# Kernel tuning notes

Measured on AMD Instinct MI355X. Metric: run time of the kernel, lower is better.

The kernel has to match this reference:

```python
import jax, jax.numpy as jnp
import numpy as np

NUM_HEADS = 8
QWH, QWW = 8, 8
KWH, KWW = 8, 8

def _relative_position_index():
    # Swin-style relative position index, exactly as in build()
    ch, cw = np.arange(QWH), np.arange(QWW)
    cq = np.stack(np.meshgrid(ch, cw, indexing='ij')).reshape(2, -1)  # [2, qN]
    ch, cw = np.arange(KWH), np.arange(KWW)
    ck = np.stack(np.meshgrid(ch, cw, indexing='ij')).reshape(2, -1)  # [2, kN]
    rel = (cq[:, :, None] - ck[:, None, :]).transpose(1, 2, 0)        # [qN, kN, 2]
    rel[:, :, 0] += KWH - 1
    rel[:, :, 1] += KWW - 1
    rel[:, :, 0] *= QWW + KWW - 1
    return rel.sum(-1)  # [qN, kN] int

_REL_IDX = jnp.asarray(_relative_position_index())

def setup_inputs() -> dict:
    key = jax.random.key(0)
    k1, k2, k3, k4 = jax.random.split(key, 4)
    B, C = 2048, 256
    q = jax.random.normal(k1, (B, QWH, QWW, C), dtype=jnp.float32)
    k = jax.random.normal(k2, (B, KWH, KWW, C), dtype=jnp.float32)
    v = jax.random.normal(k3, (B, KWH, KWW, C), dtype=jnp.float32)
    num_elements = (QWH + KWH - 1) * (QWW + KWW - 1)  # 225
    bias_table = 0.02 * jax.random.truncated_normal(
        k4, -2.0, 2.0, (num_elements, NUM_HEADS), dtype=jnp.float32)
    return {"q": q, "k": k, "v": v, "bias_table": bias_table}

def reference(q, k, v, bias_table):
    B, qWh, qWw, C = q.shape
    _, kWh, kWw, _ = k.shape
    qN, kN = qWh * qWw, kWh * kWw
    H = NUM_HEADS
    d = C // H
    scale = d ** -0.5
    # [B, N, H, d] -> [B, H, N, d]
    qh = q.reshape(B, qN, H, d).transpose(0, 2, 1, 3) * scale
    kh = k.reshape(B, kN, H, d).transpose(0, 2, 1, 3)
    vh = v.reshape(B, kN, H, d).transpose(0, 2, 1, 3)
    attn = jnp.einsum('bhqd,bhkd->bhqk', qh, kh)
    # gather relative-position bias: [qN, kN, H] -> [1, H, qN, kN]
    bias = bias_table[_REL_IDX].transpose(2, 0, 1)[None]
    attn = jax.nn.softmax(attn + bias, axis=-1)
    # bhqk,bhkd -> bqhd then merge heads back to channels
    x = jnp.einsum('bhqk,bhkd->bqhd', attn, vh).reshape(B, qWh, qWw, C)
    return x, attn
```

## Files before the change

kernel.cpp:

```cpp
#include <hip/hip_runtime.h>


#define NUM_HEADS 8

typedef __attribute__((ext_vector_type(8))) short bf16x8;
typedef __attribute__((ext_vector_type(4))) float f32x4;

__device__ inline unsigned cvt_pk_bf16(float lo, float hi) {
    unsigned r;
    asm("v_cvt_pk_bf16_f32 %0, %1, %2" : "=v"(r) : "v"(lo), "v"(hi));
    return r;
}

__global__ __launch_bounds__(256) void spatial_attn_mfma(
    const float* __restrict__ q,
    const float* __restrict__ k,
    const float* __restrict__ v,
    const float* __restrict__ bias_table,
    float* __restrict__ x_out,
    float* __restrict__ attn_out)
{
    __shared__ short q_lds[64 * 32];
    __shared__ short k_lds[64 * 32];
    __shared__ short vt_lds[32 * 64];
    __shared__ short p_lds[64 * 64];
    __shared__ float attn_lds[64 * 64];
    __shared__ float bias_s[225];

    const int bh  = blockIdx.x;
    const int b   = bh >> 3;
    const int h   = bh & 7;
    const int tid = threadIdx.x;
    const int lane = tid & 63;
    const int w    = tid >> 6;

    constexpr float LOG2E  = 1.4426950408889634f;
    constexpr float SCALE2 = 0.17677669529663687f * 1.4426950408889634f;
    const size_t base = ((size_t)b * 64) * 256 + h * 32;

    #pragma unroll
    for (int it = 0; it < 2; ++it) {
        const int i   = tid + it * 256;
        const int r   = i >> 3;
        const int d4  = (i & 7) * 4;
        const size_t off = base + (size_t)r * 256 + d4;
        const f32x4 qv = __builtin_nontemporal_load((const f32x4*)(q + off));
        const f32x4 kv = __builtin_nontemporal_load((const f32x4*)(k + off));
        const f32x4 vv = __builtin_nontemporal_load((const f32x4*)(v + off));

        const int u  = d4 >> 3;
        const int so = r * 32 + ((u ^ ((r >> 1) & 3)) << 3) + (d4 & 7);
        uint2 qb, kb;
        qb.x = cvt_pk_bf16(qv[0] * SCALE2, qv[1] * SCALE2);
        qb.y = cvt_pk_bf16(qv[2] * SCALE2, qv[3] * SCALE2);
        kb.x = cvt_pk_bf16(kv[0], kv[1]);
        kb.y = cvt_pk_bf16(kv[2], kv[3]);
        *(uint2*)(&q_lds[so]) = qb;
        *(uint2*)(&k_lds[so]) = kb;

        const unsigned vb0 = cvt_pk_bf16(vv[0], vv[1]);
        const unsigned vb1 = cvt_pk_bf16(vv[2], vv[3]);
        const int ur = r >> 3, rl = r & 7;
        vt_lds[(d4+0)*64 + ((ur ^ ((d4+0)&7)) << 3) + rl] = (short)vb0;
        vt_lds[(d4+1)*64 + ((ur ^ ((d4+1)&7)) << 3) + rl] = (short)(vb0 >> 16);
        vt_lds[(d4+2)*64 + ((ur ^ ((d4+2)&7)) << 3) + rl] = (short)vb1;
        vt_lds[(d4+3)*64 + ((ur ^ ((d4+3)&7)) << 3) + rl] = (short)(vb1 >> 16);
    }
    for (int i = tid; i < 225; i += 256)
        bias_s[i] = bias_table[i * NUM_HEADS + h] * LOG2E;
    __syncthreads();

    const int lr = lane & 15;
    const int lg = lane >> 4;
    const int arow = 16 * w + lr;
    const bf16x8 a_frag =
        *(const bf16x8*)(&q_lds[arow * 32 + ((lg ^ ((arow >> 1) & 3)) << 3)]);

    const int crow_base = 16 * w + lg * 4;

    f32x4 acc[4];
    {
        const int lrh = lr >> 3, lrl = lr & 7;
        #pragma unroll
        for (int j = 0; j < 4; ++j) {
            const int e  = 4 * lg + j;
            const int bj = (2 * w + (e >> 3) - lrh + 7) * 15 + (e & 7) - lrl + 7;
            #pragma unroll
            for (int t = 0; t < 4; ++t) acc[t][j] = bias_s[bj - 30 * t];
        }
    }
    #pragma unroll
    for (int t = 0; t < 4; ++t) {
        const int krow = 16 * t + lr;
        const bf16x8 b_frag =
            *(const bf16x8*)(&k_lds[krow * 32 + ((lg ^ ((krow >> 1) & 3)) << 3)]);
        acc[t] = __builtin_amdgcn_mfma_f32_16x16x32_bf16(a_frag, b_frag, acc[t], 0, 0, 0);
    }

    #pragma unroll
    for (int j = 0; j < 4; ++j) {
        const int rr = crow_base + j;
        float e0 = __builtin_amdgcn_exp2f(acc[0][j]);
        float e1 = __builtin_amdgcn_exp2f(acc[1][j]);
        float e2 = __builtin_amdgcn_exp2f(acc[2][j]);
        float e3 = __builtin_amdgcn_exp2f(acc[3][j]);
        float s = (e0 + e1) + (e2 + e3);
        s += __shfl_xor(s, 1);
        s += __shfl_xor(s, 2);
        s += __shfl_xor(s, 4);
        s += __shfl_xor(s, 8);
        const float inv = __builtin_amdgcn_rcpf(s);
        e0 *= inv; e1 *= inv; e2 *= inv; e3 *= inv;

        const int rb64 = rr * 64, rot = 4 * rr;
        attn_lds[rb64 + ((lr      + rot) & 63)] = e0;
        attn_lds[rb64 + ((16 + lr + rot) & 63)] = e1;
        attn_lds[rb64 + ((32 + lr + rot) & 63)] = e2;
        attn_lds[rb64 + ((48 + lr + rot) & 63)] = e3;

        const unsigned p01 = cvt_pk_bf16(e0, e1);
        const unsigned p23 = cvt_pk_bf16(e2, e3);
        const int rsw = rr & 7, rb = rr * 64, cl = lr & 7, ch = (lr >> 3);
        p_lds[rb + (((0 + ch) ^ rsw) << 3) + cl] = (short)p01;
        p_lds[rb + (((2 + ch) ^ rsw) << 3) + cl] = (short)(p01 >> 16);
        p_lds[rb + (((4 + ch) ^ rsw) << 3) + cl] = (short)p23;
        p_lds[rb + (((6 + ch) ^ rsw) << 3) + cl] = (short)(p23 >> 16);
    }

    const size_t attn_base = (size_t)bh * 64 * 64;
    #pragma unroll
    for (int j2 = 0; j2 < 4; ++j2) {
        const int rr = 16 * w + 4 * j2 + (lane >> 4);
        const int c0 = 4 * (lane & 15);
        const f32x4 av = *(const f32x4*)(&attn_lds[rr * 64 + ((c0 + 4 * rr) & 63)]);
        __builtin_nontemporal_store(av,
            (f32x4*)(attn_out + attn_base + (size_t)rr * 64 + c0));
    }

    f32x4 o[2] = {};
    const int prow = 16 * w + lr;
    #pragma unroll
    for (int s = 0; s < 2; ++s) {
        const int unit = s * 4 + lg;
        const bf16x8 pa =
            *(const bf16x8*)(&p_lds[prow * 64 + ((unit ^ (prow & 7)) << 3)]);
        #pragma unroll
        for (int t = 0; t < 2; ++t) {
            const int c = 16 * t + lr;
            const bf16x8 vb =
                *(const bf16x8*)(&vt_lds[c * 64 + ((unit ^ (c & 7)) << 3)]);
            o[t] = __builtin_amdgcn_mfma_f32_16x16x32_bf16(pa, vb, o[t], 0, 0, 0);
        }
    }

    {
        float* xs = attn_lds + 16 * w * 64;
        #pragma unroll
        for (int t = 0; t < 2; ++t) {
            #pragma unroll
            for (int j = 0; j < 4; ++j) {
                const int rr = crow_base + j;
                xs[(rr & 15) * 32 + ((16 * t + lr + 4 * rr) & 31)] = o[t][j];
            }
        }
        #pragma unroll
        for (int j3 = 0; j3 < 2; ++j3) {
            const int rr = 16 * w + 8 * j3 + (lane >> 3);
            const int c0 = 4 * (lane & 7);
            const f32x4 xv = *(const f32x4*)(&xs[(rr & 15) * 32 + ((c0 + 4 * rr) & 31)]);
            __builtin_nontemporal_store(xv,
                (f32x4*)(x_out + base + (size_t)rr * 256 + c0));
        }
    }
}

extern "C" void kernel_launch(void* const* d_in, const int* in_sizes, int n_in,
                              void* d_out, int out_size, void* d_ws, size_t ws_size,
                              hipStream_t stream) {
    const float* q    = (const float*)d_in[0];
    const float* k    = (const float*)d_in[1];
    const float* v    = (const float*)d_in[2];
    const float* bias = (const float*)d_in[3];

    const int B = in_sizes[0] / (8 * 8 * 256);
    float* x_out    = (float*)d_out;
    float* attn_out = x_out + (size_t)B * 64 * 256;

    spatial_attn_mfma<<<dim3(B * NUM_HEADS), dim3(256), 0, stream>>>(
        q, k, v, bias, x_out, attn_out);
}
```

Baseline: 159.9 us.

## Shrink LDS footprint, load Q fragments directly, reuse shared buffer for staging

Drops the Q and attn LDS buffers. Each lane now loads its own Q MFMA A-fragment from global memory and converts it to bf16 in registers. Softmax results stay in the accumulator registers and are staged for the coalesced attn and x stores through one aliased 17 KB shared buffer, after an added barrier. The smaller LDS footprint plus launch_bounds(256,6) is meant to raise occupancy so more memory traffic is in flight, at the cost of an extra __syncthreads and more register pressure.

After: 165.6 us. +3.6%, slower.

```diff
diff --git a/kernel.cpp b/kernel.cpp
--- a/kernel.cpp
+++ b/kernel.cpp
@@ -4,6 +4,7 @@
 #define NUM_HEADS 8
 
 typedef __attribute__((ext_vector_type(8))) short bf16x8;
+typedef __attribute__((ext_vector_type(4))) unsigned u32x4;
 typedef __attribute__((ext_vector_type(4))) float f32x4;
 
 __device__ inline unsigned cvt_pk_bf16(float lo, float hi) {
@@ -12,7 +13,7 @@
     return r;
 }
 
-__global__ __launch_bounds__(256) void spatial_attn_mfma(
+__global__ __launch_bounds__(256, 6) void spatial_attn_mfma(
     const float* __restrict__ q,
     const float* __restrict__ k,
     const float* __restrict__ v,
@@ -20,12 +21,11 @@
     float* __restrict__ x_out,
     float* __restrict__ attn_out)
 {
-    __shared__ short q_lds[64 * 32];
-    __shared__ short k_lds[64 * 32];
-    __shared__ short vt_lds[32 * 64];
-    __shared__ short p_lds[64 * 64];
-    __shared__ float attn_lds[64 * 64];
-    __shared__ float bias_s[225];
+    __shared__ __attribute__((aligned(16))) char smem[17408];
+    short* k_lds  = (short*)smem;
+    short* p_lds  = (short*)(smem + 4096);
+    short* vt_lds = (short*)(smem + 12288);
+    float* bias_s = (float*)(smem + 16384);
 
     const int bh  = blockIdx.x;
     const int b   = bh >> 3;
@@ -33,10 +33,18 @@
     const int tid = threadIdx.x;
     const int lane = tid & 63;
     const int w    = tid >> 6;
+    const int lr   = lane & 15;
+    const int lg   = lane >> 4;
 
     constexpr float LOG2E  = 1.4426950408889634f;
     constexpr float SCALE2 = 0.17677669529663687f * 1.4426950408889634f;
     const size_t base = ((size_t)b * 64) * 256 + h * 32;
+
+    const int qrow = 16 * w + lr;
+    const f32x4 qr0 = __builtin_nontemporal_load(
+        (const f32x4*)(q + base + (size_t)qrow * 256 + 8 * lg));
+    const f32x4 qr1 = __builtin_nontemporal_load(
+        (const f32x4*)(q + base + (size_t)qrow * 256 + 8 * lg + 4));
 
     #pragma unroll
     for (int it = 0; it < 2; ++it) {
@@ -44,18 +52,14 @@
         const int r   = i >> 3;
         const int d4  = (i & 7) * 4;
         const size_t off = base + (size_t)r * 256 + d4;
-        const f32x4 qv = __builtin_nontemporal_load((const f32x4*)(q + off));
         const f32x4 kv = __builtin_nontemporal_load((const f32x4*)(k + off));
         const f32x4 vv = __builtin_nontemporal_load((const f32x4*)(v + off));
 
         const int u  = d4 >> 3;
         const int so = r * 32 + ((u ^ ((r >> 1) & 3)) << 3) + (d4 & 7);
-        uint2 qb, kb;
-        qb.x = cvt_pk_bf16(qv[0] * SCALE2, qv[1] * SCALE2);
-        qb.y = cvt_pk_bf16(qv[2] * SCALE2, qv[3] * SCALE2);
+        uint2 kb;
         kb.x = cvt_pk_bf16(kv[0], kv[1]);
         kb.y = cvt_pk_bf16(kv[2], kv[3]);
-        *(uint2*)(&q_lds[so]) = qb;
         *(uint2*)(&k_lds[so]) = kb;
 
         const unsigned vb0 = cvt_pk_bf16(vv[0], vv[1]);
@@ -68,13 +72,15 @@
     }
     for (int i = tid; i < 225; i += 256)
         bias_s[i] = bias_table[i * NUM_HEADS + h] * LOG2E;
+
+    u32x4 afu;
+    afu[0] = cvt_pk_bf16(qr0[0] * SCALE2, qr0[1] * SCALE2);
+    afu[1] = cvt_pk_bf16(qr0[2] * SCALE2, qr0[3] * SCALE2);
+    afu[2] = cvt_pk_bf16(qr1[0] * SCALE2, qr1[1] * SCALE2);
+    afu[3] = cvt_pk_bf16(qr1[2] * SCALE2, qr1[3] * SCALE2);
+    const bf16x8 a_frag = __builtin_bit_cast(bf16x8, afu);
+
     __syncthreads();
-
-    const int lr = lane & 15;
-    const int lg = lane >> 4;
-    const int arow = 16 * w + lr;
-    const bf16x8 a_frag =
-        *(const bf16x8*)(&q_lds[arow * 32 + ((lg ^ ((arow >> 1) & 3)) << 3)]);
 
     const int crow_base = 16 * w + lg * 4;
 
@@ -111,12 +117,7 @@
         s += __shfl_xor(s, 8);
         const float inv = __builtin_amdgcn_rcpf(s);
         e0 *= inv; e1 *= inv; e2 *= inv; e3 *= inv;
-
-        const int rb64 = rr * 64, rot = 4 * rr;
-        attn_lds[rb64 + ((lr      + rot) & 63)] = e0;
-        attn_lds[rb64 + ((16 + lr + rot) & 63)] = e1;
-        attn_lds[rb64 + ((32 + lr + rot) & 63)] = e2;
-        attn_lds[rb64 + ((48 + lr + rot) & 63)] = e3;
+        acc[0][j] = e0; acc[1][j] = e1; acc[2][j] = e2; acc[3][j] = e3;
 
         const unsigned p01 = cvt_pk_bf16(e0, e1);
         const unsigned p23 = cvt_pk_bf16(e2, e3);
@@ -127,23 +128,14 @@
         p_lds[rb + (((6 + ch) ^ rsw) << 3) + cl] = (short)(p23 >> 16);
     }
 
-    const size_t attn_base = (size_t)bh * 64 * 64;
-    #pragma unroll
-    for (int j2 = 0; j2 < 4; ++j2) {
-        const int rr = 16 * w + 4 * j2 + (lane >> 4);
-        const int c0 = 4 * (lane & 15);
-        const f32x4 av = *(const f32x4*)(&attn_lds[rr * 64 + ((c0 + 4 * rr) & 63)]);
-        __builtin_nontemporal_store(av,
-            (f32x4*)(attn_out + attn_base + (size_t)rr * 64 + c0));
-    }
-
     f32x4 o[2] = {};
     const int prow = 16 * w + lr;
     #pragma unroll
     for (int s = 0; s < 2; ++s) {
         const int unit = s * 4 + lg;
         const bf16x8 pa =
-            *(const bf16x8*)(&p_lds[prow * 64 + ((unit ^ (prow & 7)) << 3)]);
+            *(const bf16x8*)(&p_lds[prow * 128 + ((unit ^ (prow & 7)) << 3)
+                             - prow * 64]);
         #pragma unroll
         for (int t = 0; t < 2; ++t) {
             const int c = 16 * t + lr;
@@ -153,24 +145,46 @@
         }
     }
 
-    {
-        float* xs = attn_lds + 16 * w * 64;
+    __syncthreads();
+
+    float* stg = (float*)(smem + 4096 * w);
+    const size_t attn_base = (size_t)bh * 64 * 64;
+    #pragma unroll
+    for (int j = 0; j < 4; ++j) {
+        const int rr = crow_base + j;
+        const int rl = rr & 15, rb64 = rl * 64, rot = 4 * rr;
+        stg[rb64 + ((lr      + rot) & 63)] = acc[0][j];
+        stg[rb64 + ((16 + lr + rot) & 63)] = acc[1][j];
+        stg[rb64 + ((32 + lr + rot) & 63)] = acc[2][j];
+        stg[rb64 + ((48 + lr + rot) & 63)] = acc[3][j];
+    }
+    #pragma unroll
+    for (int j2 = 0; j2 < 4; ++j2) {
+        const int rl2 = 4 * j2 + (lane >> 4);
+        const int rr2 = 16 * w + rl2;
+        const int c0  = 4 * (lane & 15);
+        const f32x4 av = *(const f32x4*)(&stg[rl2 * 64 + ((c0 + 4 * rr2) & 63)]);
+        __builtin_nontemporal_store(av,
+            (f32x4*)(attn_out + attn_base + (size_t)rr2 * 64 + c0));
+    }
+
+    #pragma unroll
+    for (int t = 0; t < 2; ++t) {
         #pragma unroll
-        for (int t = 0; t < 2; ++t) {
-            #pragma unroll
-            for (int j = 0; j < 4; ++j) {
-                const int rr = crow_base + j;
-                xs[(rr & 15) * 32 + ((16 * t + lr + 4 * rr) & 31)] = o[t][j];
-            }
+        for (int j = 0; j < 4; ++j) {
+            const int rr = crow_base + j;
+            const int rl = rr & 15;
+            stg[rl * 32 + ((16 * t + lr + 4 * rr) & 31)] = o[t][j];
         }
-        #pragma unroll
-        for (int j3 = 0; j3 < 2; ++j3) {
-            const int rr = 16 * w + 8 * j3 + (lane >> 3);
-            const int c0 = 4 * (lane & 7);
-            const f32x4 xv = *(const f32x4*)(&xs[(rr & 15) * 32 + ((c0 + 4 * rr) & 31)]);
-            __builtin_nontemporal_store(xv,
-                (f32x4*)(x_out + base + (size_t)rr * 256 + c0));
-        }
+    }
+    #pragma unroll
+    for (int j3 = 0; j3 < 2; ++j3) {
+        const int rl3 = 8 * j3 + (lane >> 3);
+        const int rr3 = 16 * w + rl3;
+        const int c0x = 4 * (lane & 7);
+        const f32x4 xv = *(const f32x4*)(&stg[rl3 * 32 + ((c0x + 4 * rr3) & 31)]);
+        __builtin_nontemporal_store(xv,
+            (f32x4*)(x_out + base + (size_t)rr3 * 256 + c0x));
     }
 }
 
```

## Process four heads per block to widen contiguous global row accesses

Applied to the files above, without the earlier changes.

Each block now handles four heads of one batch element instead of one, so the grid shrinks from B*8 to B*2 blocks. Each block loads and stores 512-byte contiguous row segments of q, k, v and x, instead of 128-byte segments, and loops over heads with staging buffers reused per wave. The intent is better coalescing and less per-block setup overhead on a memory-bound kernel. In exchange, shared memory grows to about 77 KB per block, which cuts how many blocks fit on a CU and reduces latency hiding. Per-head work is also serialised inside each block.

Result: no change. 157.3 us (-1.7%).

```diff
diff --git a/kernel.cpp b/kernel.cpp
--- a/kernel.cpp
+++ b/kernel.cpp
@@ -20,157 +20,174 @@
     float* __restrict__ x_out,
     float* __restrict__ attn_out)
 {
-    __shared__ short q_lds[64 * 32];
-    __shared__ short k_lds[64 * 32];
-    __shared__ short vt_lds[32 * 64];
-    __shared__ short p_lds[64 * 64];
-    __shared__ float attn_lds[64 * 64];
-    __shared__ float bias_s[225];
-
-    const int bh  = blockIdx.x;
-    const int b   = bh >> 3;
-    const int h   = bh & 7;
-    const int tid = threadIdx.x;
+    __shared__ __attribute__((aligned(16))) char smem[77328];
+    short* q4         = (short*)smem;
+    short* k4         = (short*)(smem + 16384);
+    short* vt4        = (short*)(smem + 32768);
+    short* p_lds      = (short*)(smem + 49152);
+    float* attn_stage = (float*)(smem + 57344);
+    float* bias4      = (float*)(smem + 73728);
+    float* xs         = (float*)smem;
+
+    const int bid  = blockIdx.x;
+    const int b    = bid >> 1;
+    const int h0   = (bid & 1) * 4;
+    const int tid  = threadIdx.x;
     const int lane = tid & 63;
     const int w    = tid >> 6;
+    const int lr   = lane & 15;
+    const int lg   = lane >> 4;
 
     constexpr float LOG2E  = 1.4426950408889634f;
     constexpr float SCALE2 = 0.17677669529663687f * 1.4426950408889634f;
-    const size_t base = ((size_t)b * 64) * 256 + h * 32;
-
-    #pragma unroll
-    for (int it = 0; it < 2; ++it) {
-        const int i   = tid + it * 256;
-        const int r   = i >> 3;
-        const int d4  = (i & 7) * 4;
-        const size_t off = base + (size_t)r * 256 + d4;
+    const size_t hw_base = (size_t)b * 16384 + h0 * 32;
+
+    #pragma unroll
+    for (int it = 0; it < 8; ++it) {
+        const int idx = tid + it * 256;
+        const int r   = idx >> 5;
+        const int c4  = (idx & 31) * 4;
+        const size_t off = hw_base + (size_t)r * 256 + c4;
         const f32x4 qv = __builtin_nontemporal_load((const f32x4*)(q + off));
         const f32x4 kv = __builtin_nontemporal_load((const f32x4*)(k + off));
         const f32x4 vv = __builtin_nontemporal_load((const f32x4*)(v + off));
 
-        const int u  = d4 >> 3;
-        const int so = r * 32 + ((u ^ ((r >> 1) & 3)) << 3) + (d4 & 7);
+        const int hh = c4 >> 5;
+        const int dd = c4 & 31;
+        const int u  = dd >> 3;
+        const int so = hh * 2048 + r * 32 + ((u ^ ((r >> 1) & 3)) << 3) + (dd & 7);
         uint2 qb, kb;
         qb.x = cvt_pk_bf16(qv[0] * SCALE2, qv[1] * SCALE2);
         qb.y = cvt_pk_bf16(qv[2] * SCALE2, qv[3] * SCALE2);
         kb.x = cvt_pk_bf16(kv[0], kv[1]);
         kb.y = cvt_pk_bf16(kv[2], kv[3]);
-        *(uint2*)(&q_lds[so]) = qb;
-        *(uint2*)(&k_lds[so]) = kb;
+        *(uint2*)(&q4[so]) = qb;
+        *(uint2*)(&k4[so]) = kb;
 
         const unsigned vb0 = cvt_pk_bf16(vv[0], vv[1]);
         const unsigned vb1 = cvt_pk_bf16(vv[2], vv[3]);
         const int ur = r >> 3, rl = r & 7;
-        vt_lds[(d4+0)*64 + ((ur ^ ((d4+0)&7)) << 3) + rl] = (short)vb0;
-        vt_lds[(d4+1)*64 + ((ur ^ ((d4+1)&7)) << 3) + rl] = (short)(vb0 >> 16);
-        vt_lds[(d4+2)*64 + ((ur ^ ((d4+2)&7)) << 3) + rl] = (short)vb1;
-        vt_lds[(d4+3)*64 + ((ur ^ ((d4+3)&7)) << 3) + rl] = (short)(vb1 >> 16);
-    }
-    for (int i = tid; i < 225; i += 256)
-        bias_s[i] = bias_table[i * NUM_HEADS + h] * LOG2E;
+        short* vtb = vt4 + hh * 2048;
+        vtb[(dd+0)*64 + ((ur ^ ((dd+0)&7)) << 3) + rl] = (short)vb0;
+        vtb[(dd+1)*64 + ((ur ^ ((dd+1)&7)) << 3) + rl] = (short)(vb0 >> 16);
+        vtb[(dd+2)*64 + ((ur ^ ((dd+2)&7)) << 3) + rl] = (short)vb1;
+        vtb[(dd+3)*64 + ((ur ^ ((dd+3)&7)) << 3) + rl] = (short)(vb1 >> 16);
+    }
+    #pragma unroll
+    for (int hh = 0; hh < 4; ++hh)
+        for (int i = tid; i < 225; i += 256)
+            bias4[hh * 225 + i] = bias_table[i * NUM_HEADS + h0 + hh] * LOG2E;
     __syncthreads();
 
-    const int lr = lane & 15;
-    const int lg = lane >> 4;
-    const int arow = 16 * w + lr;
-    const bf16x8 a_frag =
-        *(const bf16x8*)(&q_lds[arow * 32 + ((lg ^ ((arow >> 1) & 3)) << 3)]);
-
+    const int arow      = 16 * w + lr;
     const int crow_base = 16 * w + lg * 4;
-
-    f32x4 acc[4];
-    {
-        const int lrh = lr >> 3, lrl = lr & 7;
+    const int lrh = lr >> 3, lrl = lr & 7;
+    f32x4 o[4][2] = {};
+
+    #pragma unroll
+    for (int hh = 0; hh < 4; ++hh) {
+        const short* qh = q4 + hh * 2048;
+        const short* kh = k4 + hh * 2048;
+        const short* vh = vt4 + hh * 2048;
+        const float* bs = bias4 + hh * 225;
+
+        const bf16x8 a_frag =
+            *(const bf16x8*)(&qh[arow * 32 + ((lg ^ ((arow >> 1) & 3)) << 3)]);
+
+        f32x4 acc[4];
         #pragma unroll
         for (int j = 0; j < 4; ++j) {
             const int e  = 4 * lg + j;
             const int bj = (2 * w + (e >> 3) - lrh + 7) * 15 + (e & 7) - lrl + 7;
             #pragma unroll
-            for (int t = 0; t < 4; ++t) acc[t][j] = bias_s[bj - 30 * t];
-        }
-    }
-    #pragma unroll
-    for (int t = 0; t < 4; ++t) {
-        const int krow = 16 * t + lr;
-        const bf16x8 b_frag =
-            *(const bf16x8*)(&k_lds[krow * 32 + ((lg ^ ((krow >> 1) & 3)) << 3)]);
-        acc[t] = __builtin_amdgcn_mfma_f32_16x16x32_bf16(a_frag, b_frag, acc[t], 0, 0, 0);
-    }
-
-    #pragma unroll
-    for (int j = 0; j < 4; ++j) {
-        const int rr = crow_base + j;
-        float e0 = __builtin_amdgcn_exp2f(acc[0][j]);
-        float e1 = __builtin_amdgcn_exp2f(acc[1][j]);
-        float e2 = __builtin_amdgcn_exp2f(acc[2][j]);
-        float e3 = __builtin_amdgcn_exp2f(acc[3][j]);
-        float s = (e0 + e1) + (e2 + e3);
-        s += __shfl_xor(s, 1);
-        s += __shfl_xor(s, 2);
-        s += __shfl_xor(s, 4);
-        s += __shfl_xor(s, 8);
-        const float inv = __builtin_amdgcn_rcpf(s);
-        e0 *= inv; e1 *= inv; e2 *= inv; e3 *= inv;
-
-        const int rb64 = rr * 64, rot = 4 * rr;
-        attn_lds[rb64 + ((lr      + rot) & 63)] = e0;
-        attn_lds[rb64 + ((16 + lr + rot) & 63)] = e1;
-        attn_lds[rb64 + ((32 + lr + rot) & 63)] = e2;
-        attn_lds[rb64 + ((48 + lr + rot) & 63)] = e3;
-
-        const unsigned p01 = cvt_pk_bf16(e0, e1);
-        const unsigned p23 = cvt_pk_bf16(e2, e3);
-        const int rsw = rr & 7, rb = rr * 64, cl = lr & 7, ch = (lr >> 3);
-        p_lds[rb + (((0 + ch) ^ rsw) << 3) + cl] = (short)p01;
-        p_lds[rb + (((2 + ch) ^ rsw) << 3) + cl] = (short)(p01 >> 16);
-        p_lds[rb + (((4 + ch) ^ rsw) << 3) + cl] = (short)p23;
-        p_lds[rb + (((6 + ch) ^ rsw) << 3) + cl] = (short)(p23 >> 16);
-    }
-
-    const size_t attn_base = (size_t)bh * 64 * 64;
-    #pragma unroll
-    for (int j2 = 0; j2 < 4; ++j2) {
-        const int rr = 16 * w + 4 * j2 + (lane >> 4);
-        const int c0 = 4 * (lane & 15);
-        const f32x4 av = *(const f32x4*)(&attn_lds[rr * 64 + ((c0 + 4 * rr) & 63)]);
-        __builtin_nontemporal_store(av,
-            (f32x4*)(attn_out + attn_base + (size_t)rr * 64 + c0));
-    }
-
-    f32x4 o[2] = {};
-    const int prow = 16 * w + lr;
-    #pragma unroll
-    for (int s = 0; s < 2; ++s) {
-        const int unit = s * 4 + lg;
-        const bf16x8 pa =
-            *(const bf16x8*)(&p_lds[prow * 64 + ((unit ^ (prow & 7)) << 3)]);
-        #pragma unroll
-        for (int t = 0; t < 2; ++t) {
-            const int c = 16 * t + lr;
-            const bf16x8 vb =
-                *(const bf16x8*)(&vt_lds[c * 64 + ((unit ^ (c & 7)) << 3)]);
-            o[t] = __builtin_amdgcn_mfma_f32_16x16x32_bf16(pa, vb, o[t], 0, 0, 0);
-        }
-    }
-
-    {
-        float* xs = attn_lds + 16 * w * 64;
+            for (int t = 0; t < 4; ++t) acc[t][j] = bs[bj - 30 * t];
+        }
+        #pragma unroll
+        for (int t = 0; t < 4; ++t) {
+            const int krow = 16 * t + lr;
+            const bf16x8 b_frag =
+                *(const bf16x8*)(&kh[krow * 32 + ((lg ^ ((krow >> 1) & 3)) << 3)]);
+            acc[t] = __builtin_amdgcn_mfma_f32_16x16x32_bf16(a_frag, b_frag, acc[t], 0, 0, 0);
+        }
+
+        #pragma unroll
+        for (int j = 0; j < 4; ++j) {
+            const int rr = crow_base + j;
+            float e0 = __builtin_amdgcn_exp2f(acc[0][j]);
+            float e1 = __builtin_amdgcn_exp2f(acc[1][j]);
+            float e2 = __builtin_amdgcn_exp2f(acc[2][j]);
+            float e3 = __builtin_amdgcn_exp2f(acc[3][j]);
+            float s = (e0 + e1) + (e2 + e3);
+            s += __shfl_xor(s, 1);
+            s += __shfl_xor(s, 2);
+            s += __shfl_xor(s, 4);
+            s += __shfl_xor(s, 8);
+            const float inv = __builtin_amdgcn_rcpf(s);
+            e0 *= inv; e1 *= inv; e2 *= inv; e3 *= inv;
+
+            const int rb64 = rr * 64, rot = 4 * rr;
+            attn_stage[rb64 + ((lr      + rot) & 63)] = e0;
+            attn_stage[rb64 + ((16 + lr + rot) & 63)] = e1;
+            attn_stage[rb64 + ((32 + lr + rot) & 63)] = e2;
+            attn_stage[rb64 + ((48 + lr + rot) & 63)] = e3;
+
+            const unsigned p01 = cvt_pk_bf16(e0, e1);
+            const unsigned p23 = cvt_pk_bf16(e2, e3);
+            const int rsw = rr & 7, rb = rr * 64, cl = lr & 7, ch = (lr >> 3);
+            p_lds[rb + (((0 + ch) ^ rsw) << 3) + cl] = (short)p01;
+            p_lds[rb + (((2 + ch) ^ rsw) << 3) + cl] = (short)(p01 >> 16);
+            p_lds[rb + (((4 + ch) ^ rsw) << 3) + cl] = (short)p23;
+            p_lds[rb + (((6 + ch) ^ rsw) << 3) + cl] = (short)(p23 >> 16);
+        }
+
+        const size_t attn_base = ((size_t)(b * NUM_HEADS + h0 + hh)) * 4096;
+        #pragma unroll
+        for (int j2 = 0; j2 < 4; ++j2) {
+            const int rr = 16 * w + 4 * j2 + (lane >> 4);
+            const int c0 = 4 * (lane & 15);
+            const f32x4 av = *(const f32x4*)(&attn_stage[rr * 64 + ((c0 + 4 * rr) & 63)]);
+            __builtin_nontemporal_store(av,
+                (f32x4*)(attn_out + attn_base + (size_t)rr * 64 + c0));
+        }
+
+        const int prow = 16 * w + lr;
+        #pragma unroll
+        for (int s = 0; s < 2; ++s) {
+            const int unit = s * 4 + lg;
+            const bf16x8 pa =
+                *(const bf16x8*)(&p_lds[prow * 64 + ((unit ^ (prow & 7)) << 3)]);
+            #pragma unroll
+            for (int t = 0; t < 2; ++t) {
+                const int c = 16 * t + lr;
+                const bf16x8 vb =
+                    *(const bf16x8*)(&vh[c * 64 + ((unit ^ (c & 7)) << 3)]);
+                o[hh][t] = __builtin_amdgcn_mfma_f32_16x16x32_bf16(pa, vb, o[hh][t], 0, 0, 0);
+            }
+        }
+    }
+
+    __syncthreads();
+
+    #pragma unroll
+    for (int hh = 0; hh < 4; ++hh) {
         #pragma unroll
         for (int t = 0; t < 2; ++t) {
             #pragma unroll
             for (int j = 0; j < 4; ++j) {
                 const int rr = crow_base + j;
-                xs[(rr & 15) * 32 + ((16 * t + lr + 4 * rr) & 31)] = o[t][j];
+                const int c  = hh * 32 + 16 * t + lr;
+                xs[rr * 128 + ((c + 4 * rr) & 127)] = o[hh][t][j];
             }
         }
-        #pragma unroll
-        for (int j3 = 0; j3 < 2; ++j3) {
-            const int rr = 16 * w + 8 * j3 + (lane >> 3);
-            const int c0 = 4 * (lane & 7);
-            const f32x4 xv = *(const f32x4*)(&xs[(rr & 15) * 32 + ((c0 + 4 * rr) & 31)]);
-            __builtin_nontemporal_store(xv,
-                (f32x4*)(x_out + base + (size_t)rr * 256 + c0));
-        }
+    }
+    #pragma unroll
+    for (int m = 0; m < 8; ++m) {
+        const int idx2 = (w * 8 + m) * 64 + lane;
+        const int r    = idx2 >> 5;
+        const int c4   = (idx2 & 31) * 4;
+        const f32x4 xv = *(const f32x4*)(&xs[r * 128 + ((c4 + 4 * r) & 127)]);
+        __builtin_nontemporal_store(xv,
+            (f32x4*)(x_out + hw_base + (size_t)r * 256 + c4));
     }
 }
 
@@ -186,6 +203,6 @@
     float* x_out    = (float*)d_out;
     float* attn_out = x_out + (size_t)B * 64 * 256;
 
-    spatial_attn_mfma<<<dim3(B * NUM_HEADS), dim3(256), 0, stream>>>(
+    spatial_attn_mfma<<<dim3(B * 2), dim3(256), 0, stream>>>(
         q, k, v, bias, x_out, attn_out);
 }
```
